# Optimization experiments

Measured on AMD Instinct MI355X. Metric: run time of the kernel, lower is better.

The kernel has to match this reference:

```python
import jax, jax.numpy as jnp
import numpy as np

DIM = 768
HEADS = 12
HEAD_DIM = 64
INNER = HEADS * HEAD_DIM  # 768


def setup_inputs() -> dict:
    key = jax.random.key(0)
    k_x, k_wqkv, k_bqkv, k_wout, k_bout = jax.random.split(key, 5)
    B, S = 2, 2048
    x = jax.random.normal(k_x, (B, S, DIM), dtype=jnp.float32)
    # nn.Linear(dim, 3*inner): weight [out, in]; store transposed for x @ W
    lim = 1.0 / np.sqrt(DIM)
    w_qkv = jax.random.uniform(k_wqkv, (DIM, 3 * INNER), minval=-lim, maxval=lim, dtype=jnp.float32)
    b_qkv = jax.random.uniform(k_bqkv, (3 * INNER,), minval=-lim, maxval=lim, dtype=jnp.float32)
    lim2 = 1.0 / np.sqrt(INNER)
    # original zero-inits to_out; use random weights so the reference output is non-trivial
    w_out = jax.random.uniform(k_wout, (INNER, DIM), minval=-lim2, maxval=lim2, dtype=jnp.float32)
    b_out = jax.random.uniform(k_bout, (DIM,), minval=-lim2, maxval=lim2, dtype=jnp.float32)
    return {"x": x, "w_qkv": w_qkv, "b_qkv": b_qkv, "w_out": w_out, "b_out": b_out}


def reference(x, w_qkv, b_qkv, w_out, b_out):
    B, S, _ = x.shape
    qkv = x @ w_qkv + b_qkv                               # [B, S, 3*H*D]
    qkv = qkv.reshape(B, S, 3, HEADS, HEAD_DIM)           # b s three h d
    q, k, v = qkv[:, :, 0], qkv[:, :, 1], qkv[:, :, 2]    # each [B, S, H, D]
    scale = 1.0 / np.sqrt(HEAD_DIM)
    # non-causal self-attention (FlashSelfAttention, dropout=0, causal=False)
    scores = jnp.einsum('bshd,bthd->bhst', q, k) * scale  # [B, H, S, S]
    attn = jax.nn.softmax(scores, axis=-1)
    ctx = jnp.einsum('bhst,bthd->bshd', attn, v)          # [B, S, H, D]
    ctx = ctx.reshape(B, S, INNER)
    return ctx @ w_out + b_out                            # [B, S, DIM]
```

## Files before the change

kernel.cpp:

```cpp
#include <hip/hip_runtime.h>
#include <cstddef>
#include <cstdint>

#define DIM  768
#define NH   12
#define HD   64
#define SEQ  2048
#define NB   2
#define NQKV 2304
#define G    (NB * NH * SEQ)

typedef _Float16 f16x8 __attribute__((ext_vector_type(8)));
typedef _Float16 f16x4 __attribute__((ext_vector_type(4)));
typedef __fp16   h16x2 __attribute__((ext_vector_type(2)));
typedef float    f32x4 __attribute__((ext_vector_type(4)));
typedef float    f32x16 __attribute__((ext_vector_type(16)));

#if __has_builtin(__builtin_amdgcn_exp2f)
#define EXP2(x) __builtin_amdgcn_exp2f(x)
#else
#define EXP2(x) exp2f(x)
#endif

#define QSCALE 0.1803368801111244f

__device__ __forceinline__ int pkrtz_i(float a, float b) {
  union { h16x2 h; int w; } u;
  u.h = __builtin_amdgcn_cvt_pkrtz(a, b);
  return u.w;
}

__global__ __launch_bounds__(256) void transpose_cvt_kernel(
    const float* __restrict__ W, _Float16* __restrict__ WT, int K, int N) {
  __shared__ _Float16 tl[32][36];
  const int t = threadIdx.x;
  const int k0 = blockIdx.y * 32, n0 = blockIdx.x * 32;
  {
    const int r = t >> 3, c4 = (t & 7) * 4;
    float4 f = *(const float4*)(W + (size_t)(k0 + r) * N + n0 + c4);
    tl[r][c4 + 0] = (_Float16)f.x; tl[r][c4 + 1] = (_Float16)f.y;
    tl[r][c4 + 2] = (_Float16)f.z; tl[r][c4 + 3] = (_Float16)f.w;
  }
  __syncthreads();
  const int n = t >> 3, kc = (t & 7) * 4;
  f16x4 v;
  v[0] = tl[kc + 0][n]; v[1] = tl[kc + 1][n];
  v[2] = tl[kc + 2][n]; v[3] = tl[kc + 3][n];
  *(f16x4*)(WT + (size_t)(n0 + n) * K + k0 + kc) = v;
}

__global__ __launch_bounds__(256) void vtrans_kernel(
    const _Float16* __restrict__ v, _Float16* __restrict__ vT) {
  __shared__ _Float16 tl[64][68];
  const int t = threadIdx.x;
  const int bh = blockIdx.x, st = blockIdx.y;
  const size_t base = (size_t)bh * SEQ * HD;
  {
    const int s = t >> 2, dc = (t & 3) * 16;
    const _Float16* p = v + base + (size_t)(st * 64 + s) * HD + dc;
    f16x8 a = *(const f16x8*)p, b = *(const f16x8*)(p + 8);
    *(f16x8*)&tl[s][dc] = a;
    *(f16x8*)&tl[s][dc + 8] = b;
  }
  __syncthreads();
  const int d = t >> 2, sc = (t & 3) * 16;
  f16x8 o0, o1;
#pragma unroll
  for (int j = 0; j < 8; j++) { o0[j] = tl[sc + j][d]; o1[j] = tl[sc + 8 + j][d]; }
  _Float16* q = vT + base + (size_t)d * SEQ + st * 64 + sc;
  *(f16x8*)q = o0;
  *(f16x8*)(q + 8) = o1;
}

#define QKV_STEPS (DIM / 32)
__global__ __launch_bounds__(256, 2) void qkv_gemm_kernel(
    const float* __restrict__ X, const _Float16* __restrict__ BT,
    const float* __restrict__ bias, _Float16* __restrict__ q,
    _Float16* __restrict__ k, _Float16* __restrict__ v) {
  __shared__ _Float16 As[2][128 * 32];
  __shared__ _Float16 Bs[2][128 * 32];
  const int tid = threadIdx.x;
  const int lane = tid & 63, wv = tid >> 6;
  const int wm = wv >> 1, wn = wv & 1;
  const int quad = lane >> 4, lcol = lane & 15;
  const int bm = blockIdx.y * 128, bn = blockIdx.x * 128;
  const int K = DIM;

  f32x4 acc[4][4];
#pragma unroll
  for (int i = 0; i < 4; i++)
#pragma unroll
    for (int j = 0; j < 4; j++) acc[i][j] = (f32x4)(0.f);

  const float* asrc[2];
  int aoff[2];
#pragma unroll
  for (int i = 0; i < 2; i++) {
    const int rA = 64 * i + (tid >> 2);
    const int cc = tid & 3;
    asrc[i] = X + (size_t)(bm + rA) * K + cc * 8;
    aoff[i] = rA * 32 + ((cc ^ ((rA >> 1) & 3)) * 8);
  }
  const int r0 = wv * 32 + (lane >> 2);
  const int kpos = (((lane & 3) ^ ((r0 >> 1) & 3)) * 8);
  const _Float16* b0p = BT + (size_t)(bn + r0) * K + kpos;
  const _Float16* b1p = BT + (size_t)(bn + r0 + 16) * K + kpos;
  const int boff0 = r0 * 32 + (lane & 3) * 8;
  const int boff1 = (r0 + 16) * 32 + (lane & 3) * 8;

  float4 a0[2], a1[2];
  f16x8 br0, br1;
#pragma unroll
  for (int i = 0; i < 2; i++) {
    a0[i] = *(const float4*)(asrc[i]);
    a1[i] = *(const float4*)(asrc[i] + 4);
  }
  br0 = *(const f16x8*)b0p;
  br1 = *(const f16x8*)b1p;
#pragma unroll
  for (int i = 0; i < 2; i++) {
    f16x8 h;
    h[0] = (_Float16)a0[i].x; h[1] = (_Float16)a0[i].y;
    h[2] = (_Float16)a0[i].z; h[3] = (_Float16)a0[i].w;
    h[4] = (_Float16)a1[i].x; h[5] = (_Float16)a1[i].y;
    h[6] = (_Float16)a1[i].z; h[7] = (_Float16)a1[i].w;
    *(f16x8*)&As[0][aoff[i]] = h;
  }
  *(f16x8*)&Bs[0][boff0] = br0;
  *(f16x8*)&Bs[0][boff1] = br1;
#pragma unroll
  for (int i = 0; i < 2; i++) {
    a0[i] = *(const float4*)(asrc[i] + 32);
    a1[i] = *(const float4*)(asrc[i] + 32 + 4);
  }
  br0 = *(const f16x8*)(b0p + 32);
  br1 = *(const f16x8*)(b1p + 32);
  asm volatile("s_waitcnt lgkmcnt(0)" ::: "memory");

  for (int t = 0; t < QKV_STEPS; t++) {
    const int cur = t & 1;
    __builtin_amdgcn_s_barrier();
    __builtin_amdgcn_sched_barrier(0);

    f16x8 af[4], bf[4];
#pragma unroll
    for (int mi = 0; mi < 4; mi++) {
      const int R = wm * 64 + mi * 16 + lcol;
      af[mi] = *(const f16x8*)&As[cur][R * 32 + ((quad ^ ((R >> 1) & 3)) * 8)];
    }
#pragma unroll
    for (int ni = 0; ni < 4; ni++) {
      const int R = wn * 64 + ni * 16 + lcol;
      bf[ni] = *(const f16x8*)&Bs[cur][R * 32 + ((quad ^ ((R >> 1) & 3)) * 8)];
    }
    __builtin_amdgcn_s_setprio(1);
#pragma unroll
    for (int mi = 0; mi < 4; mi++)
#pragma unroll
      for (int ni = 0; ni < 4; ni++)
        acc[mi][ni] = __builtin_amdgcn_mfma_f32_16x16x32_f16(af[mi], bf[ni], acc[mi][ni], 0, 0, 0);
    __builtin_amdgcn_s_setprio(0);

    if (t + 1 < QKV_STEPS) {
      const int nxt = cur ^ 1;
#pragma unroll
      for (int i = 0; i < 2; i++) {
        f16x8 h;
        h[0] = (_Float16)a0[i].x; h[1] = (_Float16)a0[i].y;
        h[2] = (_Float16)a0[i].z; h[3] = (_Float16)a0[i].w;
        h[4] = (_Float16)a1[i].x; h[5] = (_Float16)a1[i].y;
        h[6] = (_Float16)a1[i].z; h[7] = (_Float16)a1[i].w;
        *(f16x8*)&As[nxt][aoff[i]] = h;
      }
      *(f16x8*)&Bs[nxt][boff0] = br0;
      *(f16x8*)&Bs[nxt][boff1] = br1;
      if (t + 2 < QKV_STEPS) {
        const int k2 = (t + 2) * 32;
#pragma unroll
        for (int i = 0; i < 2; i++) {
          a0[i] = *(const float4*)(asrc[i] + k2);
          a1[i] = *(const float4*)(asrc[i] + k2 + 4);
        }
        br0 = *(const f16x8*)(b0p + k2);
        br1 = *(const f16x8*)(b1p + k2);
      }
      asm volatile("s_waitcnt lgkmcnt(0)" ::: "memory");
    }
  }

#pragma unroll
  for (int mi = 0; mi < 4; mi++) {
#pragma unroll
    for (int r = 0; r < 4; r++) {
      const int row = bm + wm * 64 + mi * 16 + quad * 4 + r;
      const int b_ = row >> 11, s_ = row & 2047;
#pragma unroll
      for (int ni = 0; ni < 4; ni++) {
        const int c = bn + wn * 64 + ni * 16 + lcol;
        const float val = acc[mi][ni][r] + bias[c];
        const int d = c & 63;
        const int which = c / 768;
        const int h = (c - which * 768) >> 6;
        const size_t idx = (((size_t)b_ * NH + h) * SEQ + s_) * HD + d;
        if (which == 0)      q[idx] = (_Float16)(val * QSCALE);
        else if (which == 1) k[idx] = (_Float16)val;
        else                 v[idx] = (_Float16)val;
      }
    }
  }
}

#define PST 68
#define KSPLIT 2
#define KEYS (SEQ / KSPLIT)
#define TILES (KEYS / 64)
__global__ __launch_bounds__(256, 2) void attn_part_kernel(
    const _Float16* __restrict__ Q, const _Float16* __restrict__ K,
    const _Float16* __restrict__ V, _Float16* __restrict__ Ohat,
    float* __restrict__ L) {
  __shared__ _Float16 Ks[2][64 * PST];
  __shared__ _Float16 Vs[2][64 * PST];
  __shared__ float lsh[4][2][32];
  const int tid = threadIdx.x, lane = tid & 63, wv = tid >> 6;
  const int lr = lane & 31, hw = lane >> 5;
  const int bh = blockIdx.x, qt = blockIdx.y, ks = blockIdx.z;
  const size_t base = (size_t)bh * SEQ * HD;

  f16x8 qb[2][4];
#pragma unroll
  for (int qs = 0; qs < 2; qs++) {
    const _Float16* qp =
        Q + base + (size_t)(qt * 256 + wv * 64 + qs * 32 + lr) * HD + hw * 8;
#pragma unroll
    for (int f = 0; f < 4; f++) qb[qs][f] = *(const f16x8*)(qp + f * 16);
  }

  f32x16 o00 = (f32x16)(0.f), o01 = (f32x16)(0.f);
  f32x16 o10 = (f32x16)(0.f), o11 = (f32x16)(0.f);
  float lpa0 = 0.f, lpb0 = 0.f, lpa1 = 0.f, lpb1 = 0.f;

  const int sr = tid >> 2;
  const int sc = (tid & 3) * 16;
  const _Float16* kp = K + base + (size_t)ks * KEYS * HD + (size_t)sr * HD + sc;
  const _Float16* vp = V + base + ks * KEYS + (size_t)sr * SEQ + sc;

  f16x8 kr0 = *(const f16x8*)kp, kr1 = *(const f16x8*)(kp + 8);
  f16x8 vr0 = *(const f16x8*)vp, vr1 = *(const f16x8*)(vp + 8);
  *(f16x8*)&Ks[0][sr * PST + sc]     = kr0;
  *(f16x8*)&Ks[0][sr * PST + sc + 8] = kr1;
  *(f16x8*)&Vs[0][sr * PST + sc]     = vr0;
  *(f16x8*)&Vs[0][sr * PST + sc + 8] = vr1;
  kr0 = *(const f16x8*)(kp + 64 * HD); kr1 = *(const f16x8*)(kp + 64 * HD + 8);
  vr0 = *(const f16x8*)(vp + 64);      vr1 = *(const f16x8*)(vp + 64 + 8);
  asm volatile("s_waitcnt lgkmcnt(0)" ::: "memory");

  for (int t = 0; t < TILES; t++) {
    const int cur = t & 1;
    __builtin_amdgcn_s_barrier();
    __builtin_amdgcn_sched_barrier(0);

    f16x8 ka0[4], ka1[4];
#pragma unroll
    for (int f = 0; f < 4; f++) {
      ka0[f] = *(const f16x8*)&Ks[cur][lr * PST + f * 16 + hw * 8];
      ka1[f] = *(const f16x8*)&Ks[cur][(32 + lr) * PST + f * 16 + hw * 8];
    }

    f32x16 s00 = (f32x16)(0.f), s01 = (f32x16)(0.f);
    f32x16 s10 = (f32x16)(0.f), s11 = (f32x16)(0.f);
    __builtin_amdgcn_s_setprio(1);
#pragma unroll
    for (int f = 0; f < 4; f++) {
      s00 = __builtin_amdgcn_mfma_f32_32x32x16_f16(ka0[f], qb[0][f], s00, 0, 0, 0);
      s01 = __builtin_amdgcn_mfma_f32_32x32x16_f16(ka1[f], qb[0][f], s01, 0, 0, 0);
      s10 = __builtin_amdgcn_mfma_f32_32x32x16_f16(ka0[f], qb[1][f], s10, 0, 0, 0);
      s11 = __builtin_amdgcn_mfma_f32_32x32x16_f16(ka1[f], qb[1][f], s11, 0, 0, 0);
    }
    __builtin_amdgcn_s_setprio(0);

    f16x8 pf0[4], pf1[4];
#pragma unroll
    for (int f = 0; f < 4; f++) {
      const f32x16& sv = (f < 2) ? s00 : s01;
      const int r0 = (f & 1) * 8;
      const float e0 = EXP2(sv[r0 + 0]), e1 = EXP2(sv[r0 + 1]);
      const float e2 = EXP2(sv[r0 + 2]), e3 = EXP2(sv[r0 + 3]);
      const float e4 = EXP2(sv[r0 + 4]), e5 = EXP2(sv[r0 + 5]);
      const float e6 = EXP2(sv[r0 + 6]), e7 = EXP2(sv[r0 + 7]);
      lpa0 += (e0 + e1) + (e2 + e3);
      lpb0 += (e4 + e5) + (e6 + e7);
      const int a01 = pkrtz_i(e0, e1), b45 = pkrtz_i(e4, e5);
      const int c23 = pkrtz_i(e2, e3), d67 = pkrtz_i(e6, e7);
      auto w02 = __builtin_amdgcn_permlane32_swap(a01, b45, false, false);
      auto w13 = __builtin_amdgcn_permlane32_swap(c23, d67, false, false);
      union { f16x8 h; int w[4]; } pu;
      pu.w[0] = w02[0]; pu.w[1] = w13[0]; pu.w[2] = w02[1]; pu.w[3] = w13[1];
      pf0[f] = pu.h;
    }
#pragma unroll
    for (int f = 0; f < 4; f++) {
      const f32x16& sv = (f < 2) ? s10 : s11;
      const int r0 = (f & 1) * 8;
      const float e0 = EXP2(sv[r0 + 0]), e1 = EXP2(sv[r0 + 1]);
      const float e2 = EXP2(sv[r0 + 2]), e3 = EXP2(sv[r0 + 3]);
      const float e4 = EXP2(sv[r0 + 4]), e5 = EXP2(sv[r0 + 5]);
      const float e6 = EXP2(sv[r0 + 6]), e7 = EXP2(sv[r0 + 7]);
      lpa1 += (e0 + e1) + (e2 + e3);
      lpb1 += (e4 + e5) + (e6 + e7);
      const int a01 = pkrtz_i(e0, e1), b45 = pkrtz_i(e4, e5);
      const int c23 = pkrtz_i(e2, e3), d67 = pkrtz_i(e6, e7);
      auto w02 = __builtin_amdgcn_permlane32_swap(a01, b45, false, false);
      auto w13 = __builtin_amdgcn_permlane32_swap(c23, d67, false, false);
      union { f16x8 h; int w[4]; } pu;
      pu.w[0] = w02[0]; pu.w[1] = w13[0]; pu.w[2] = w02[1]; pu.w[3] = w13[1];
      pf1[f] = pu.h;
    }

    __builtin_amdgcn_s_setprio(1);
#pragma unroll
    for (int f = 0; f < 4; f++) {
      f16x8 vb0 = *(const f16x8*)&Vs[cur][lr * PST + f * 16 + hw * 8];
      f16x8 vb1 = *(const f16x8*)&Vs[cur][(32 + lr) * PST + f * 16 + hw * 8];
      o00 = __builtin_amdgcn_mfma_f32_32x32x16_f16(pf0[f], vb0, o00, 0, 0, 0);
      o01 = __builtin_amdgcn_mfma_f32_32x32x16_f16(pf0[f], vb1, o01, 0, 0, 0);
      o10 = __builtin_amdgcn_mfma_f32_32x32x16_f16(pf1[f], vb0, o10, 0, 0, 0);
      o11 = __builtin_amdgcn_mfma_f32_32x32x16_f16(pf1[f], vb1, o11, 0, 0, 0);
    }
    __builtin_amdgcn_s_setprio(0);

    if (t + 1 < TILES) {
      const int nxt = cur ^ 1;
      *(f16x8*)&Ks[nxt][sr * PST + sc]     = kr0;
      *(f16x8*)&Ks[nxt][sr * PST + sc + 8] = kr1;
      *(f16x8*)&Vs[nxt][sr * PST + sc]     = vr0;
      *(f16x8*)&Vs[nxt][sr * PST + sc + 8] = vr1;
      if (t + 2 < TILES) {
        const _Float16* kn = kp + (size_t)(t + 2) * 64 * HD;
        const _Float16* vn = vp + (t + 2) * 64;
        kr0 = *(const f16x8*)kn; kr1 = *(const f16x8*)(kn + 8);
        vr0 = *(const f16x8*)vn; vr1 = *(const f16x8*)(vn + 8);
      }
      asm volatile("s_waitcnt lgkmcnt(0)" ::: "memory");
    }
  }

  float l0 = lpa0 + lpb0; l0 += __shfl_xor(l0, 32);
  float l1 = lpa1 + lpb1; l1 += __shfl_xor(l1, 32);
  __syncthreads();
  if (hw == 0) { lsh[wv][0][lr] = l0; lsh[wv][1][lr] = l1; }
  __syncthreads();

#pragma unroll
  for (int qs = 0; qs < 2; qs++) {
    const f32x16& oa = qs ? o10 : o00;
    const f32x16& ob = qs ? o11 : o01;
    const size_t rbase =
        (size_t)ks * G + (size_t)bh * SEQ + qt * 256 + wv * 64 + qs * 32;
    if (hw == 0) L[rbase + lr] = qs ? l1 : l0;
    float linv[16];
#pragma unroll
    for (int r = 0; r < 16; r++)
      linv[r] = 1.00048828125f / lsh[wv][qs][(r & 3) + 8 * (r >> 2) + 4 * hw];
#pragma unroll
    for (int r = 0; r < 16; r++) {
      const int rr = (r & 3) + 8 * (r >> 2) + 4 * hw;
      _Float16* cp = Ohat + (rbase + rr) * HD;
      cp[lr]      = (_Float16)(oa[r] * linv[r]);
      cp[32 + lr] = (_Float16)(ob[r] * linv[r]);
    }
  }
}

__global__ __launch_bounds__(256) void out_gemm_kernel(
    const _Float16* __restrict__ Ohat, const float* __restrict__ L,
    const _Float16* __restrict__ WT, const float* __restrict__ bias,
    float* __restrict__ out) {
  __shared__ _Float16 As[64 * 36];
  __shared__ _Float16 Bs[64 * 36];
  const int tid = threadIdx.x, lane = tid & 63, wv = tid >> 6;
  const int wr = (wv >> 1) * 32, wc = (wv & 1) * 32;
  const int quad = lane >> 4, lcol = lane & 15;
  const int bm = blockIdx.y * 64, bn = blockIdx.x * 64;

  f32x4 acc[2][2];
#pragma unroll
  for (int i = 0; i < 2; i++)
#pragma unroll
    for (int j = 0; j < 2; j++) acc[i][j] = (f32x4)(0.f);

  const int ra = tid >> 2, ca = (tid & 3) * 8;
  const int grow = bm + ra, b_ = grow >> 11, s_ = grow & 2047;

  for (int k0 = 0; k0 < DIM; k0 += 32) {
    const int h = k0 >> 6;
    const int lidx = (b_ * NH + h) * SEQ + s_;
    const size_t obase = (size_t)lidx * HD + (k0 & 32) + ca;
    f16x8 u0 = *(const f16x8*)(Ohat + obase);
    f16x8 u1 = *(const f16x8*)(Ohat + (size_t)G * HD + obase);
    const float l0 = L[lidx], l1 = L[G + lidx];
    const float w0 = l0 / (l0 + l1), w1 = 1.0f - w0;
    f16x8 bv = *(const f16x8*)(WT + (size_t)(bn + ra) * DIM + k0 + ca);

    __syncthreads();
    f16x8 av;
#pragma unroll
    for (int j = 0; j < 8; j++)
      av[j] = (_Float16)(w0 * (float)u0[j] + w1 * (float)u1[j]);
    *(f16x8*)&As[ra * 36 + ca] = av;
    *(f16x8*)&Bs[ra * 36 + ca] = bv;
    __syncthreads();

    f16x8 af[2], bf[2];
#pragma unroll
    for (int mi = 0; mi < 2; mi++)
      af[mi] = *(const f16x8*)&As[(wr + mi * 16 + lcol) * 36 + quad * 8];
#pragma unroll
    for (int ni = 0; ni < 2; ni++)
      bf[ni] = *(const f16x8*)&Bs[(wc + ni * 16 + lcol) * 36 + quad * 8];
#pragma unroll
    for (int mi = 0; mi < 2; mi++)
#pragma unroll
      for (int ni = 0; ni < 2; ni++)
        acc[mi][ni] = __builtin_amdgcn_mfma_f32_16x16x32_f16(af[mi], bf[ni], acc[mi][ni], 0, 0, 0);
  }

#pragma unroll
  for (int mi = 0; mi < 2; mi++) {
#pragma unroll
    for (int r = 0; r < 4; r++) {
      const int row = bm + wr + mi * 16 + quad * 4 + r;
#pragma unroll
      for (int ni = 0; ni < 2; ni++) {
        const int col = bn + wc + ni * 16 + lcol;
        out[(size_t)row * DIM + col] = acc[mi][ni][r] + bias[col];
      }
    }
  }
}

extern "C" void kernel_launch(void* const* d_in, const int* in_sizes, int n_in,
                              void* d_out, int out_size, void* d_ws,
                              size_t ws_size, hipStream_t stream) {
  const float* x = (const float*)d_in[0];
  const float* w_qkv = (const float*)d_in[1];
  const float* b_qkv = (const float*)d_in[2];
  const float* w_out = (const float*)d_in[3];
  const float* b_out = (const float*)d_in[4];
  float* out = (float*)d_out;

  _Float16* wsh = (_Float16*)d_ws;
  size_t off = 0;
  const size_t hsz = (size_t)NB * NH * SEQ * HD;
  _Float16* wqkvT = wsh + off; off += (size_t)NQKV * DIM;
  _Float16* woutT = wsh + off; off += (size_t)DIM * DIM;
  _Float16* qh   = wsh + off; off += hsz;
  _Float16* kh   = wsh + off; off += hsz;
  _Float16* vh   = wsh + off; off += hsz;
  _Float16* vT   = wsh + off; off += hsz;
  _Float16* Ohat = wsh + off; off += 2 * hsz;
  float*    Lbuf = (float*)(wsh + off);

  transpose_cvt_kernel<<<dim3(NQKV / 32, DIM / 32), 256, 0, stream>>>(w_qkv, wqkvT, DIM, NQKV);
  transpose_cvt_kernel<<<dim3(DIM / 32, DIM / 32), 256, 0, stream>>>(w_out, woutT, DIM, DIM);
  qkv_gemm_kernel<<<dim3(NQKV / 128, (NB * SEQ) / 128), 256, 0, stream>>>(
      x, wqkvT, b_qkv, qh, kh, vh);
  vtrans_kernel<<<dim3(NB * NH, SEQ / 64), 256, 0, stream>>>(vh, vT);
  attn_part_kernel<<<dim3(NB * NH, SEQ / 256, KSPLIT), 256, 0, stream>>>(
      qh, kh, vT, Ohat, Lbuf);
  out_gemm_kernel<<<dim3(DIM / 64, (NB * SEQ) / 64), 256, 0, stream>>>(
      Ohat, Lbuf, woutT, b_out, out);
}
```

Baseline: 170.7 us.

## Double-buffer out-projection GEMM LDS tiles and merge weight transpose launches

The out-projection GEMM now uses double-buffered shared memory tiles with register prefetch of the next K-step's Ohat/L/weight loads, one barrier per step, and raised wave priority around MFMAs. This is meant to hide global load latency behind compute and drop one of the two barriers per step. The two weight transpose/convert kernels are also merged into one launch to save launch overhead. The cost is double the LDS use and more live registers, with launch_bounds set for 2 blocks.

```diff
diff --git a/kernel.cpp b/kernel.cpp
--- a/kernel.cpp
+++ b/kernel.cpp
@@ -30,11 +30,23 @@
   return u.w;
 }
 
-__global__ __launch_bounds__(256) void transpose_cvt_kernel(
-    const float* __restrict__ W, _Float16* __restrict__ WT, int K, int N) {
+#define CVT_BLOCKS0 ((NQKV / 32) * (DIM / 32))
+#define CVT_BLOCKS1 ((DIM / 32) * (DIM / 32))
+__global__ __launch_bounds__(256) void transpose_cvt2_kernel(
+    const float* __restrict__ W0, _Float16* __restrict__ WT0,
+    const float* __restrict__ W1, _Float16* __restrict__ WT1) {
   __shared__ _Float16 tl[32][36];
+  const int bid = blockIdx.x;
+  const float* W; _Float16* WT; int N, bx, by;
+  if (bid < CVT_BLOCKS0) {
+    W = W0; WT = WT0; N = NQKV; bx = bid % (NQKV / 32); by = bid / (NQKV / 32);
+  } else {
+    const int b2 = bid - CVT_BLOCKS0;
+    W = W1; WT = WT1; N = DIM; bx = b2 % (DIM / 32); by = b2 / (DIM / 32);
+  }
+  const int K = DIM;
   const int t = threadIdx.x;
-  const int k0 = blockIdx.y * 32, n0 = blockIdx.x * 32;
+  const int k0 = by * 32, n0 = bx * 32;
   {
     const int r = t >> 3, c4 = (t & 7) * 4;
     float4 f = *(const float4*)(W + (size_t)(k0 + r) * N + n0 + c4);
@@ -371,12 +383,13 @@
   }
 }
 
-__global__ __launch_bounds__(256) void out_gemm_kernel(
+#define OUT_STEPS (DIM / 32)
+__global__ __launch_bounds__(256, 2) void out_gemm_kernel(
     const _Float16* __restrict__ Ohat, const float* __restrict__ L,
     const _Float16* __restrict__ WT, const float* __restrict__ bias,
     float* __restrict__ out) {
-  __shared__ _Float16 As[64 * 36];
-  __shared__ _Float16 Bs[64 * 36];
+  __shared__ _Float16 As[2][64 * 36];
+  __shared__ _Float16 Bs[2][64 * 36];
   const int tid = threadIdx.x, lane = tid & 63, wv = tid >> 6;
   const int wr = (wv >> 1) * 32, wc = (wv & 1) * 32;
   const int quad = lane >> 4, lcol = lane & 15;
@@ -390,38 +403,79 @@
 
   const int ra = tid >> 2, ca = (tid & 3) * 8;
   const int grow = bm + ra, b_ = grow >> 11, s_ = grow & 2047;
-
-  for (int k0 = 0; k0 < DIM; k0 += 32) {
-    const int h = k0 >> 6;
-    const int lidx = (b_ * NH + h) * SEQ + s_;
-    const size_t obase = (size_t)lidx * HD + (k0 & 32) + ca;
-    f16x8 u0 = *(const f16x8*)(Ohat + obase);
-    f16x8 u1 = *(const f16x8*)(Ohat + (size_t)G * HD + obase);
+  const int aoff = ra * 36 + ca;
+  const _Float16* wtp = WT + (size_t)(bn + ra) * DIM + ca;
+
+  f16x8 u0, u1, bv;
+  float w0, w1;
+  {
+    const int lidx = (b_ * NH + 0) * SEQ + s_;
+    const size_t obase = (size_t)lidx * HD + ca;
+    u0 = *(const f16x8*)(Ohat + obase);
+    u1 = *(const f16x8*)(Ohat + (size_t)G * HD + obase);
     const float l0 = L[lidx], l1 = L[G + lidx];
-    const float w0 = l0 / (l0 + l1), w1 = 1.0f - w0;
-    f16x8 bv = *(const f16x8*)(WT + (size_t)(bn + ra) * DIM + k0 + ca);
-
-    __syncthreads();
+    w0 = l0 / (l0 + l1); w1 = 1.0f - w0;
+    bv = *(const f16x8*)wtp;
     f16x8 av;
 #pragma unroll
     for (int j = 0; j < 8; j++)
       av[j] = (_Float16)(w0 * (float)u0[j] + w1 * (float)u1[j]);
-    *(f16x8*)&As[ra * 36 + ca] = av;
-    *(f16x8*)&Bs[ra * 36 + ca] = bv;
-    __syncthreads();
+    *(f16x8*)&As[0][aoff] = av;
+    *(f16x8*)&Bs[0][aoff] = bv;
+  }
+  {
+    const int k0 = 32;
+    const int lidx = (b_ * NH + 0) * SEQ + s_;
+    const size_t obase = (size_t)lidx * HD + 32 + ca;
+    u0 = *(const f16x8*)(Ohat + obase);
+    u1 = *(const f16x8*)(Ohat + (size_t)G * HD + obase);
+    const float l0 = L[lidx], l1 = L[G + lidx];
+    w0 = l0 / (l0 + l1); w1 = 1.0f - w0;
+    bv = *(const f16x8*)(wtp + k0);
+  }
+  asm volatile("s_waitcnt lgkmcnt(0)" ::: "memory");
+
+  for (int t = 0; t < OUT_STEPS; t++) {
+    const int cur = t & 1;
+    __builtin_amdgcn_s_barrier();
+    __builtin_amdgcn_sched_barrier(0);
 
     f16x8 af[2], bf[2];
 #pragma unroll
     for (int mi = 0; mi < 2; mi++)
-      af[mi] = *(const f16x8*)&As[(wr + mi * 16 + lcol) * 36 + quad * 8];
+      af[mi] = *(const f16x8*)&As[cur][(wr + mi * 16 + lcol) * 36 + quad * 8];
 #pragma unroll
     for (int ni = 0; ni < 2; ni++)
-      bf[ni] = *(const f16x8*)&Bs[(wc + ni * 16 + lcol) * 36 + quad * 8];
+      bf[ni] = *(const f16x8*)&Bs[cur][(wc + ni * 16 + lcol) * 36 + quad * 8];
+    __builtin_amdgcn_s_setprio(1);
 #pragma unroll
     for (int mi = 0; mi < 2; mi++)
 #pragma unroll
       for (int ni = 0; ni < 2; ni++)
         acc[mi][ni] = __builtin_amdgcn_mfma_f32_16x16x32_f16(af[mi], bf[ni], acc[mi][ni], 0, 0, 0);
+    __builtin_amdgcn_s_setprio(0);
+
+    if (t + 1 < OUT_STEPS) {
+      const int nxt = cur ^ 1;
+      f16x8 av;
+#pragma unroll
+      for (int j = 0; j < 8; j++)
+        av[j] = (_Float16)(w0 * (float)u0[j] + w1 * (float)u1[j]);
+      *(f16x8*)&As[nxt][aoff] = av;
+      *(f16x8*)&Bs[nxt][aoff] = bv;
+      if (t + 2 < OUT_STEPS) {
+        const int k2 = (t + 2) * 32;
+        const int h = k2 >> 6;
+        const int lidx = (b_ * NH + h) * SEQ + s_;
+        const size_t obase = (size_t)lidx * HD + (k2 & 32) + ca;
+        u0 = *(const f16x8*)(Ohat + obase);
+        u1 = *(const f16x8*)(Ohat + (size_t)G * HD + obase);
+        const float l0 = L[lidx], l1 = L[G + lidx];
+        w0 = l0 / (l0 + l1); w1 = 1.0f - w0;
+        bv = *(const f16x8*)(wtp + k2);
+      }
+      asm volatile("s_waitcnt lgkmcnt(0)" ::: "memory");
+    }
   }
 
 #pragma unroll
@@ -460,8 +514,8 @@
   _Float16* Ohat = wsh + off; off += 2 * hsz;
   float*    Lbuf = (float*)(wsh + off);
 
-  transpose_cvt_kernel<<<dim3(NQKV / 32, DIM / 32), 256, 0, stream>>>(w_qkv, wqkvT, DIM, NQKV);
-  transpose_cvt_kernel<<<dim3(DIM / 32, DIM / 32), 256, 0, stream>>>(w_out, woutT, DIM, DIM);
+  transpose_cvt2_kernel<<<dim3(CVT_BLOCKS0 + CVT_BLOCKS1), 256, 0, stream>>>(
+      w_qkv, wqkvT, w_out, woutT);
   qkv_gemm_kernel<<<dim3(NQKV / 128, (NB * SEQ) / 128), 256, 0, stream>>>(
       x, wqkvT, b_qkv, qh, kh, vh);
   vtrans_kernel<<<dim3(NB * NH, SEQ / 64), 256, 0, stream>>>(vh, vT);
```

New measurement: 167.0 us. 2.1% less time.
